# Kernel tuning notes

Hardware: AMD Instinct MI355X
Metric: run time of the kernel (lower is better)

The kernel has to match this reference:

```python
import jax, jax.numpy as jnp
import numpy as np

EPS = 1e-12  # tf.nn.l2_normalize epsilon used by keras Dot(normalize=True)

def _l2_normalize(x):
    # x: [..., D]; matches tf.nn.l2_normalize: x * rsqrt(max(sum(x^2), eps))
    sq = jnp.sum(x * x, axis=-1, keepdims=True)
    return x * jax.lax.rsqrt(jnp.maximum(sq, EPS))

def setup_inputs() -> dict:
    key = jax.random.key(0)
    k1, k2, k3 = jax.random.split(key, 3)
    B, L, D = 16, 1024, 1024
    a = jax.random.normal(k1, (B, L, D), dtype=jnp.float32)
    b = jax.random.normal(k2, (B, L, D), dtype=jnp.float32)
    # keras 'uniform' initializer: U(-0.05, 0.05)
    kernel = jax.random.uniform(k3, (D, 1), dtype=jnp.float32, minval=-0.05, maxval=0.05)
    return {"a": a, "b": b, "kernel": kernel}

def reference(a, b, kernel):
    # kernel: [D, 1] -> broadcastable weight vector [D]
    w = kernel[:, 0]
    # elementwise kernel weighting of both sequences: [B, L, D]
    ra = _l2_normalize(a * w)
    rb = _l2_normalize(b * w)
    # cosine-similarity matrix over sequence positions: [B, L, L]
    return jnp.einsum('bid,bjd->bij', ra, rb)
```

## Files before the change

kernel.cpp:

```cpp
#include <hip/hip_runtime.h>
#include <hip/hip_bf16.h>


typedef __bf16 bf16x8 __attribute__((ext_vector_type(8)));
typedef float f32x4 __attribute__((ext_vector_type(4)));

__device__ __forceinline__ unsigned short f2bf(float f) {
  __hip_bfloat16 h = __float2bfloat16(f);
  return *reinterpret_cast<unsigned short*>(&h);
}

__device__ __forceinline__ void gload16(const void* g, void* lds) {
  __builtin_amdgcn_global_load_lds(
      (const __attribute__((address_space(1))) unsigned int*)g,
      (__attribute__((address_space(3))) unsigned int*)lds,
      16, 0, 0);
}

__global__ void __launch_bounds__(256)
norm_scale_kernel(const float* __restrict__ a, const float* __restrict__ b,
                  const float* __restrict__ w, unsigned short* __restrict__ ra,
                  unsigned short* __restrict__ rb) {
  const int wave = threadIdx.x >> 6;
  const int lane = threadIdx.x & 63;
  const int row = blockIdx.x * 4 + wave;

  const float* src;
  unsigned short* dst;
  if (row < 16384) {
    src = a + (size_t)row * 1024;
    dst = ra + (size_t)row * 1024;
  } else {
    src = b + (size_t)(row - 16384) * 1024;
    dst = rb + (size_t)(row - 16384) * 1024;
  }

  float4 x[4];
  float sq = 0.f;
#pragma unroll
  for (int c = 0; c < 4; ++c) {
    float4 xv = *(const float4*)(src + c * 256 + lane * 4);
    float4 wv = *(const float4*)(w + c * 256 + lane * 4);
    xv.x *= wv.x; xv.y *= wv.y; xv.z *= wv.z; xv.w *= wv.w;
    x[c] = xv;
    sq += xv.x * xv.x + xv.y * xv.y + xv.z * xv.z + xv.w * xv.w;
  }
#pragma unroll
  for (int off = 32; off > 0; off >>= 1) sq += __shfl_xor(sq, off);
  const float s = rsqrtf(fmaxf(sq, 1e-12f));
#pragma unroll
  for (int c = 0; c < 4; ++c) {
    ushort4 u;
    u.x = f2bf(x[c].x * s);
    u.y = f2bf(x[c].y * s);
    u.z = f2bf(x[c].z * s);
    u.w = f2bf(x[c].w * s);
    *(ushort4*)(dst + c * 256 + lane * 4) = u;
  }
}

__global__ void __launch_bounds__(256, 3)
gemm_bt_kernel(const unsigned short* __restrict__ RA,
               const unsigned short* __restrict__ RB,
               float* __restrict__ C) {
  constexpr int D = 1024;
  __shared__ char lds[32768];

  const int t = threadIdx.x;
  const int w = t >> 6;
  const int l = t & 63;
  const int wr = w >> 1, wc = w & 1;

  const int orig = (int)blockIdx.x;
  const int wgid = (orig & 7) * ((int)gridDim.x >> 3) + (orig >> 3);
  const int batch = wgid >> 6;
  const int tile = wgid & 63;
  const int brow = (tile >> 3) << 7;
  const int bcol = (tile & 7) << 7;

  const unsigned short* Ab = RA + ((size_t)batch << 20);
  const unsigned short* Bb = RB + ((size_t)batch << 20);

  const unsigned short* ga0 = Ab + (size_t)(brow + (t >> 2)) * D + (t & 3) * 8;
  const unsigned short* ga1 = ga0 + (size_t)64 * D;
  const unsigned short* gb0 = Bb + (size_t)(bcol + (t >> 2)) * D + (t & 3) * 8;
  const unsigned short* gb1 = gb0 + (size_t)64 * D;

  char* sA = (char*)lds;
  const int wA = w << 10;

  const int rdA = ((wr << 6) + (l & 15)) * 64 + ((l >> 4) << 4);
  const int rdB = 8192 + ((wc << 6) + (l & 15)) * 64 + ((l >> 4) << 4);

  f32x4 acc[4][4] = {};

#define STAGE(BOFF)                                  \
  do {                                               \
    gload16(ga0, sA + (BOFF) + wA);                  \
    gload16(ga1, sA + (BOFF) + 4096 + wA);           \
    gload16(gb0, sA + (BOFF) + 8192 + wA);           \
    gload16(gb1, sA + (BOFF) + 12288 + wA);          \
    ga0 += 32; ga1 += 32; gb0 += 32; gb1 += 32;      \
  } while (0)

  STAGE(0);
  asm volatile("s_waitcnt vmcnt(0)" ::: "memory");
  __syncthreads();

  int bufoff = 0;
#pragma unroll 1
  for (int kt = 0; kt < 31; ++kt) {
    const int nbuf = bufoff ^ 16384;
    STAGE(nbuf);

    bf16x8 af[4], bfr[4];
#pragma unroll
    for (int m = 0; m < 4; ++m)
      af[m] = *(const bf16x8*)(sA + bufoff + rdA + m * 1024);
#pragma unroll
    for (int n = 0; n < 4; ++n)
      bfr[n] = *(const bf16x8*)(sA + bufoff + rdB + n * 1024);

#pragma unroll
    for (int m = 0; m < 4; ++m)
#pragma unroll
      for (int n = 0; n < 4; ++n)
        acc[m][n] = __builtin_amdgcn_mfma_f32_16x16x32_bf16(af[m], bfr[n],
                                                            acc[m][n], 0, 0, 0);
    __syncthreads();
    bufoff = nbuf;
  }

  {
    bf16x8 af[4], bfr[4];
#pragma unroll
    for (int m = 0; m < 4; ++m)
      af[m] = *(const bf16x8*)(sA + bufoff + rdA + m * 1024);
#pragma unroll
    for (int n = 0; n < 4; ++n)
      bfr[n] = *(const bf16x8*)(sA + bufoff + rdB + n * 1024);
#pragma unroll
    for (int m = 0; m < 4; ++m)
#pragma unroll
      for (int n = 0; n < 4; ++n)
        acc[m][n] = __builtin_amdgcn_mfma_f32_16x16x32_bf16(af[m], bfr[n],
                                                            acc[m][n], 0, 0, 0);
  }
#undef STAGE

  float* Cb = C + ((size_t)batch << 20);
  const int crow0 = brow + (wr << 6) + ((l >> 4) << 2);
  const int ccol0 = bcol + (wc << 6) + (l & 15);
#pragma unroll
  for (int m = 0; m < 4; ++m)
#pragma unroll
    for (int n = 0; n < 4; ++n) {
#pragma unroll
      for (int r = 0; r < 4; ++r) {
        Cb[(size_t)(crow0 + m * 16 + r) * 1024 + ccol0 + n * 16] = acc[m][n][r];
      }
    }
}

extern "C" void kernel_launch(void* const* d_in, const int* in_sizes, int n_in,
                              void* d_out, int out_size, void* d_ws, size_t ws_size,
                              hipStream_t stream) {
  const float* a = (const float*)d_in[0];
  const float* b = (const float*)d_in[1];
  const float* w = (const float*)d_in[2];
  float* out = (float*)d_out;

  unsigned short* ra = (unsigned short*)d_ws;
  unsigned short* rb = ra + (size_t)16 * 1024 * 1024;

  norm_scale_kernel<<<8192, 256, 0, stream>>>(a, b, w, ra, rb);
  gemm_bt_kernel<<<1024, 256, 0, stream>>>(ra, rb, out);
}
```

Before: 210.1 us.

## Rewrite batched GEMM with 256x256 tiles, 8 waves, swizzled LDS and phased pipeline

Replaces the 128x128-tile, 4-wave GEMM with a 256x256-tile, 8-wave kernel that uses 128 KB of LDS, a K-step of 64 and double buffering. LDS addresses are XOR-swizzled to avoid bank conflicts, and loads are interleaved with MFMA phases, separated by barriers and s_setprio. The aim is more reuse per byte loaded and better overlap of global loads with MFMA. In exchange, the grid drops to 256 workgroups, which may underfill the CUs, and register pressure rises to 128 accumulator floats per lane.

```diff
diff --git a/kernel.cpp b/kernel.cpp
--- a/kernel.cpp
+++ b/kernel.cpp
@@ -10,10 +10,10 @@
   return *reinterpret_cast<unsigned short*>(&h);
 }
 
-__device__ __forceinline__ void gload16(const void* g, void* lds) {
+__device__ __forceinline__ void gload16(const void* g, void* ldsp) {
   __builtin_amdgcn_global_load_lds(
       (const __attribute__((address_space(1))) unsigned int*)g,
-      (__attribute__((address_space(3))) unsigned int*)lds,
+      (__attribute__((address_space(3))) unsigned int*)ldsp,
       16, 0, 0);
 }
 
@@ -59,107 +59,156 @@
   }
 }
 
-__global__ void __launch_bounds__(256, 3)
-gemm_bt_kernel(const unsigned short* __restrict__ RA,
-               const unsigned short* __restrict__ RB,
-               float* __restrict__ C) {
-  constexpr int D = 1024;
-  __shared__ char lds[32768];
+__global__ void __launch_bounds__(512, 2)
+gemm8_kernel(const unsigned short* __restrict__ RA,
+             const unsigned short* __restrict__ RB,
+             float* __restrict__ C) {
+  __shared__ __align__(16) char lds[131072];
 
   const int t = threadIdx.x;
-  const int w = t >> 6;
-  const int l = t & 63;
-  const int wr = w >> 1, wc = w & 1;
+  const int w = t >> 6, l = t & 63;
+  const int wr = w >> 2, wc = w & 3;
+  const int l4 = l & 15, lh = l >> 4;
+  const int lr = l >> 3;
+  const int lch = (l & 7) ^ lr;
 
   const int orig = (int)blockIdx.x;
-  const int wgid = (orig & 7) * ((int)gridDim.x >> 3) + (orig >> 3);
-  const int batch = wgid >> 6;
-  const int tile = wgid & 63;
-  const int brow = (tile >> 3) << 7;
-  const int bcol = (tile & 7) << 7;
-
-  const unsigned short* Ab = RA + ((size_t)batch << 20);
-  const unsigned short* Bb = RB + ((size_t)batch << 20);
-
-  const unsigned short* ga0 = Ab + (size_t)(brow + (t >> 2)) * D + (t & 3) * 8;
-  const unsigned short* ga1 = ga0 + (size_t)64 * D;
-  const unsigned short* gb0 = Bb + (size_t)(bcol + (t >> 2)) * D + (t & 3) * 8;
-  const unsigned short* gb1 = gb0 + (size_t)64 * D;
-
-  char* sA = (char*)lds;
-  const int wA = w << 10;
-
-  const int rdA = ((wr << 6) + (l & 15)) * 64 + ((l >> 4) << 4);
-  const int rdB = 8192 + ((wc << 6) + (l & 15)) * 64 + ((l >> 4) << 4);
-
-  f32x4 acc[4][4] = {};
-
-#define STAGE(BOFF)                                  \
-  do {                                               \
-    gload16(ga0, sA + (BOFF) + wA);                  \
-    gload16(ga1, sA + (BOFF) + 4096 + wA);           \
-    gload16(gb0, sA + (BOFF) + 8192 + wA);           \
-    gload16(gb1, sA + (BOFF) + 12288 + wA);          \
-    ga0 += 32; ga1 += 32; gb0 += 32; gb1 += 32;      \
+  const int wgid = (orig & 7) * 32 + (orig >> 3);
+  const int batch = wgid >> 4;
+  const int tile = wgid & 15;
+  const int brow_t = (tile >> 2) << 8;
+  const int bcol_t = (tile & 3) << 8;
+
+  const unsigned short* Ab = RA + ((size_t)batch << 20) + (size_t)brow_t * 1024;
+  const unsigned short* Bb = RB + ((size_t)batch << 20) + (size_t)bcol_t * 1024;
+
+  int aoff[2][2], boff[2][2];
+#pragma unroll
+  for (int h = 0; h < 2; ++h)
+#pragma unroll
+    for (int g = 0; g < 2; ++g) {
+      const int rr = w * 16 + g * 8 + lr;
+      const int ga = ((rr >> 6) << 7) + h * 64 + (rr & 63);
+      const int gb = ((rr >> 5) << 6) + h * 32 + (rr & 31);
+      aoff[h][g] = ga * 1024 + lch * 8;
+      boff[h][g] = gb * 1024 + lch * 8;
+    }
+  const int stgw = w * 2048;
+
+  const int arow = (wr * 64 + l4) * 128;
+  const int brow = (wc * 32 + l4) * 128;
+  int csw[2];
+  csw[0] = ((0 + lh) ^ (l & 7)) * 16;
+  csw[1] = ((4 + lh) ^ (l & 7)) * 16;
+
+  f32x4 acc[8][4] = {};
+  bf16x8 af[4][2], bq0[2][2], bq1[2][2];
+
+#define STAGE_A(h, tau)                                                   \
+  do {                                                                    \
+    char* _d = lds + ((tau) & 1) * 65536 + (h) * 16384 + stgw;            \
+    gload16(Ab + (size_t)aoff[h][0] + (size_t)(tau) * 64, _d);            \
+    gload16(Ab + (size_t)aoff[h][1] + (size_t)(tau) * 64, _d + 1024);     \
   } while (0)
-
-  STAGE(0);
+#define STAGE_B(h, tau)                                                   \
+  do {                                                                    \
+    char* _d = lds + ((tau) & 1) * 65536 + 32768 + (h) * 16384 + stgw;    \
+    gload16(Bb + (size_t)boff[h][0] + (size_t)(tau) * 64, _d);            \
+    gload16(Bb + (size_t)boff[h][1] + (size_t)(tau) * 64, _d + 1024);     \
+  } while (0)
+#define LDA(mh, bufbase)                                                  \
+  _Pragma("unroll") for (int mm = 0; mm < 4; ++mm)                        \
+  _Pragma("unroll") for (int ks = 0; ks < 2; ++ks)                        \
+      af[mm][ks] = *(const bf16x8*)((bufbase) + (mh) * 16384 + arow +     \
+                                    mm * 2048 + csw[ks]);
+#define LDB(dst, nh, bufbase)                                             \
+  _Pragma("unroll") for (int nn = 0; nn < 2; ++nn)                        \
+  _Pragma("unroll") for (int ks = 0; ks < 2; ++ks)                        \
+      dst[nn][ks] = *(const bf16x8*)((bufbase) + 32768 + (nh) * 16384 +   \
+                                     brow + nn * 2048 + csw[ks]);
+#define MQ(mh, nh, bsrc)                                                  \
+  _Pragma("unroll") for (int mm = 0; mm < 4; ++mm)                        \
+  _Pragma("unroll") for (int nn = 0; nn < 2; ++nn)                        \
+  _Pragma("unroll") for (int ks = 0; ks < 2; ++ks)                        \
+      acc[(mh) * 4 + mm][(nh) * 2 + nn] =                                 \
+          __builtin_amdgcn_mfma_f32_16x16x32_bf16(                        \
+              af[mm][ks], bsrc[nn][ks], acc[(mh) * 4 + mm][(nh) * 2 + nn],\
+              0, 0, 0);
+#define PHASE_PRE()                                                       \
+  __builtin_amdgcn_s_barrier();                                           \
+  asm volatile("s_waitcnt lgkmcnt(0)" ::: "memory");                      \
+  __builtin_amdgcn_sched_barrier(0);                                      \
+  __builtin_amdgcn_s_setprio(1)
+#define PHASE_POST()                                                      \
+  __builtin_amdgcn_s_setprio(0);                                          \
+  __builtin_amdgcn_s_barrier()
+
+  const char* b0 = lds;
+  const char* b1 = lds + 65536;
+
+  STAGE_A(0, 0); STAGE_B(0, 0); STAGE_B(1, 0); STAGE_A(1, 0);
+  STAGE_A(0, 1); STAGE_B(0, 1); STAGE_B(1, 1);
+  asm volatile("s_waitcnt vmcnt(6)" ::: "memory");
+  __builtin_amdgcn_s_barrier();
+
+#pragma unroll 1
+  for (int i = 0; i < 7; ++i) {
+    const int u = 2 * i;
+    LDA(0, b0); LDB(bq0, 0, b0); STAGE_A(1, u + 1);
+    PHASE_PRE(); MQ(0, 0, bq0); PHASE_POST();
+    LDB(bq1, 1, b0); STAGE_A(0, u + 2);
+    PHASE_PRE(); MQ(0, 1, bq1); PHASE_POST();
+    LDA(1, b0); STAGE_B(0, u + 2);
+    PHASE_PRE(); MQ(1, 1, bq1); PHASE_POST();
+    STAGE_B(1, u + 2);
+    asm volatile("s_waitcnt vmcnt(6)" ::: "memory");
+    PHASE_PRE(); MQ(1, 0, bq0); PHASE_POST();
+    LDA(0, b1); LDB(bq0, 0, b1); STAGE_A(1, u + 2);
+    PHASE_PRE(); MQ(0, 0, bq0); PHASE_POST();
+    LDB(bq1, 1, b1); STAGE_A(0, u + 3);
+    PHASE_PRE(); MQ(0, 1, bq1); PHASE_POST();
+    LDA(1, b1); STAGE_B(0, u + 3);
+    PHASE_PRE(); MQ(1, 1, bq1); PHASE_POST();
+    STAGE_B(1, u + 3);
+    asm volatile("s_waitcnt vmcnt(6)" ::: "memory");
+    PHASE_PRE(); MQ(1, 0, bq0); PHASE_POST();
+  }
+
+  LDA(0, b0); LDB(bq0, 0, b0); STAGE_A(1, 15);
+  PHASE_PRE(); MQ(0, 0, bq0); PHASE_POST();
+  LDB(bq1, 1, b0);
+  PHASE_PRE(); MQ(0, 1, bq1); PHASE_POST();
+  LDA(1, b0);
+  PHASE_PRE(); MQ(1, 1, bq1); PHASE_POST();
   asm volatile("s_waitcnt vmcnt(0)" ::: "memory");
-  __syncthreads();
-
-  int bufoff = 0;
-#pragma unroll 1
-  for (int kt = 0; kt < 31; ++kt) {
-    const int nbuf = bufoff ^ 16384;
-    STAGE(nbuf);
-
-    bf16x8 af[4], bfr[4];
-#pragma unroll
-    for (int m = 0; m < 4; ++m)
-      af[m] = *(const bf16x8*)(sA + bufoff + rdA + m * 1024);
+  PHASE_PRE(); MQ(1, 0, bq0); PHASE_POST();
+  LDA(0, b1); LDB(bq0, 0, b1);
+  PHASE_PRE(); MQ(0, 0, bq0); PHASE_POST();
+  LDB(bq1, 1, b1);
+  PHASE_PRE(); MQ(0, 1, bq1); PHASE_POST();
+  LDA(1, b1);
+  PHASE_PRE(); MQ(1, 1, bq1); PHASE_POST();
+  PHASE_PRE(); MQ(1, 0, bq0); PHASE_POST();
+
+#undef STAGE_A
+#undef STAGE_B
+#undef LDA
+#undef LDB
+#undef MQ
+#undef PHASE_PRE
+#undef PHASE_POST
+
+  float* Cb = C + ((size_t)batch << 20);
+  const int crow0 = brow_t + wr * 128 + lh * 4;
+  const int ccol0 = bcol_t + wc * 64 + l4;
+#pragma unroll
+  for (int m = 0; m < 8; ++m)
 #pragma unroll
     for (int n = 0; n < 4; ++n)
-      bfr[n] = *(const bf16x8*)(sA + bufoff + rdB + n * 1024);
-
-#pragma unroll
-    for (int m = 0; m < 4; ++m)
-#pragma unroll
-      for (int n = 0; n < 4; ++n)
-        acc[m][n] = __builtin_amdgcn_mfma_f32_16x16x32_bf16(af[m], bfr[n],
-                                                            acc[m][n], 0, 0, 0);
-    __syncthreads();
-    bufoff = nbuf;
-  }
-
-  {
-    bf16x8 af[4], bfr[4];
-#pragma unroll
-    for (int m = 0; m < 4; ++m)
-      af[m] = *(const bf16x8*)(sA + bufoff + rdA + m * 1024);
-#pragma unroll
-    for (int n = 0; n < 4; ++n)
-      bfr[n] = *(const bf16x8*)(sA + bufoff + rdB + n * 1024);
-#pragma unroll
-    for (int m = 0; m < 4; ++m)
-#pragma unroll
-      for (int n = 0; n < 4; ++n)
-        acc[m][n] = __builtin_amdgcn_mfma_f32_16x16x32_bf16(af[m], bfr[n],
-                                                            acc[m][n], 0, 0, 0);
-  }
-#undef STAGE
-
-  float* Cb = C + ((size_t)batch << 20);
-  const int crow0 = brow + (wr << 6) + ((l >> 4) << 2);
-  const int ccol0 = bcol + (wc << 6) + (l & 15);
-#pragma unroll
-  for (int m = 0; m < 4; ++m)
-#pragma unroll
-    for (int n = 0; n < 4; ++n) {
-#pragma unroll
-      for (int r = 0; r < 4; ++r) {
-        Cb[(size_t)(crow0 + m * 16 + r) * 1024 + ccol0 + n * 16] = acc[m][n][r];
-      }
-    }
+#pragma unroll
+      for (int r = 0; r < 4; ++r)
+        Cb[(size_t)(crow0 + m * 16 + r) * 1024 + ccol0 + n * 16] =
+            acc[m][n][r];
 }
 
 extern "C" void kernel_launch(void* const* d_in, const int* in_sizes, int n_in,
@@ -174,5 +223,5 @@
   unsigned short* rb = ra + (size_t)16 * 1024 * 1024;
 
   norm_scale_kernel<<<8192, 256, 0, stream>>>(a, b, w, ra, rb);
-  gemm_bt_kernel<<<1024, 256, 0, stream>>>(ra, rb, out);
-}
+  gemm8_kernel<<<256, 512, 0, stream>>>(ra, rb, out);
+}
```

Measured after the change: 204.0 us. 1.03x faster.
